# Kernel tuning notes

Measured on AMD Instinct MI355X. Metric: run time of the kernel, lower is better.

## Reference

```python
import jax, jax.numpy as jnp
import numpy as np

B, T, N, D, E = 16, 12, 512, 128, 32  # batch, time, nodes, model_dim, node_emb_dim


def setup_inputs() -> dict:
    key = jax.random.key(0)
    ks = jax.random.split(key, 7)
    return {
        "value": jax.random.normal(ks[0], (B, T, N, D), dtype=jnp.float32),
        "emb": jax.random.normal(ks[1], (T, N, E), dtype=jnp.float32),
        "attn_mask": jax.random.randint(ks[2], (B, N, N), 0, 2, dtype=jnp.int32),
        "W_qk": jax.random.normal(ks[3], (E, D), dtype=jnp.float32) * (1.0 / np.sqrt(E)),
        "b_qk": jax.random.normal(ks[4], (D,), dtype=jnp.float32) * 0.02,
        "W_v": jax.random.normal(ks[5], (D, D), dtype=jnp.float32) * (1.0 / np.sqrt(D)),
        "b_v": jax.random.normal(ks[6], (D,), dtype=jnp.float32) * 0.02,
    }


def reference(value, emb, attn_mask, W_qk, b_qk, W_v, b_v):
    # qk projection shared between query and key: [T, N, D]
    qk = emb @ W_qk + b_qk
    # query: softmax over feature dim D
    q = jax.nn.softmax(qk, axis=-1)                      # [T, N, D]
    # key: transpose then softmax over node dim N
    k = jax.nn.softmax(jnp.swapaxes(qk, -1, -2), axis=-1)  # [T, D, N]
    # value projection (note: out_proj in __init__ is unused in forward)
    v = value @ W_v + b_v                                # [B, T, N, D]
    # batch-independent base attention score, then broadcast over batch
    score = jnp.einsum('tnd,tdm->tnm', q, k)             # [T, N, N]
    score = jnp.broadcast_to(score[None], (value.shape[0],) + score.shape)  # [B, T, N, N]
    # masked fill: mask [B, N, N] -> [B, 1, N, N]
    score = jnp.where(attn_mask[:, None] == 0, jnp.float32(-1e9), score)
    out = jnp.einsum('btnm,btmd->btnd', score, v)         # [B, T, N, D]
    return out
```

## Files before the change

### kernel.cpp

```cpp
#include <hip/hip_runtime.h>

#define B_ 16
#define T_ 12
#define N_ 512
#define D_ 128
#define E_ 32

typedef __attribute__((ext_vector_type(8))) unsigned short u16x8;
typedef __attribute__((ext_vector_type(8))) __bf16 bf16x8;
typedef __attribute__((ext_vector_type(4))) float f32x4;

static __device__ __forceinline__ unsigned short f2bf(float f) {
    unsigned u = __float_as_uint(f);
    unsigned r = (u + 0x7fffu + ((u >> 16) & 1u)) >> 16;
    return (unsigned short)r;
}

static __device__ __forceinline__ void gld16(const void* src, void* dst) {
    __builtin_amdgcn_global_load_lds(
        (const __attribute__((address_space(1))) unsigned*)src,
        (__attribute__((address_space(3))) unsigned*)dst, 16, 0, 0);
}

__global__ __launch_bounds__(256) void k1(const float* __restrict__ emb,
                                          const float* __restrict__ Wqk,
                                          const float* __restrict__ bqk,
                                          unsigned short* __restrict__ qb,
                                          unsigned short* __restrict__ kN,
                                          const float* __restrict__ Wv,
                                          unsigned short* __restrict__ WvT,
                                          const int* __restrict__ mask,
                                          unsigned* __restrict__ mb) {
    __shared__ __align__(16) char LE[256 * 128];
    __shared__ float red[2][4][8];
    int hwid = blockIdx.x;
    int bid = (hwid & 7) * 144 + (hwid >> 3);
    int tid = threadIdx.x;

    if (bid < 192) {
        int t = bid >> 4;
        int d0 = (bid & 15) * 8;
        int dc = tid & 7, ni = tid >> 3;
        int wave = tid >> 6, lane = tid & 63;
        int l3 = lane >> 3, l7 = lane & 7;
        float wqv[E_];
#pragma unroll
        for (int e = 0; e < E_; ++e) wqv[e] = Wqk[e * D_ + d0 + dc];
        float bq = bqk[d0 + dc];
        const char* eb = (const char*)(emb + (size_t)t * N_ * E_);

        float vals[16];
#pragma unroll
        for (int pass = 0; pass < 2; ++pass) {
#pragma unroll
            for (int it = 0; it < 8; ++it) {
                int rl = it * 32 + wave * 8 + l3;
                int rg = pass * 256 + rl;
                gld16(eb + (size_t)rg * 128 + ((l7 * 16) ^ ((rg & 7) << 4)),
                      LE + (it * 32 + wave * 8) * 128 + lane * 16);
            }
            __syncthreads();
#pragma unroll
            for (int jj = 0; jj < 8; ++jj) {
                int n = pass * 256 + ni + 32 * jj;
                int nl = ni + 32 * jj;
                float a = bq;
#pragma unroll
                for (int s = 0; s < 8; ++s) {
                    f32x4 ev = *(const f32x4*)(LE + nl * 128 +
                                               ((s * 16) ^ ((n & 7) << 4)));
                    a = fmaf(ev[0], wqv[s * 4 + 0], a);
                    a = fmaf(ev[1], wqv[s * 4 + 1], a);
                    a = fmaf(ev[2], wqv[s * 4 + 2], a);
                    a = fmaf(ev[3], wqv[s * 4 + 3], a);
                }
                vals[pass * 8 + jj] = a;
            }
            __syncthreads();
        }

        float mx = -1e30f;
#pragma unroll
        for (int j = 0; j < 16; ++j) mx = fmaxf(mx, vals[j]);
#pragma unroll
        for (int s = 8; s < 64; s <<= 1) mx = fmaxf(mx, __shfl_xor(mx, s));
        int wv = tid >> 6;
        if ((tid & 63) < 8) red[0][wv][dc] = mx;
        __syncthreads();
        mx = fmaxf(fmaxf(red[0][0][dc], red[0][1][dc]),
                   fmaxf(red[0][2][dc], red[0][3][dc]));
        float sum = 0.f;
#pragma unroll
        for (int j = 0; j < 16; ++j) {
            vals[j] = __expf(vals[j] - mx);
            sum += vals[j];
        }
#pragma unroll
        for (int s = 8; s < 64; s <<= 1) sum += __shfl_xor(sum, s);
        if ((tid & 63) < 8) red[1][wv][dc] = sum;
        __syncthreads();
        sum = red[1][0][dc] + red[1][1][dc] + red[1][2][dc] + red[1][3][dc];
        float inv = 1.f / sum;
        unsigned short* op = kN + (size_t)t * N_ * D_ + d0 + dc;
#pragma unroll
        for (int j = 0; j < 16; ++j)
            op[(size_t)(ni + 32 * j) * D_] = f2bf(vals[j] * inv);
        return;
    }

    if (bid < 576) {
        int bid2 = bid - 192;
        int w = tid >> 6, l = tid & 63;
        float wq0[E_], wq1[E_];
#pragma unroll
        for (int e = 0; e < E_; ++e) {
            wq0[e] = Wqk[e * D_ + l];
            wq1[e] = Wqk[e * D_ + l + 64];
        }
        float b0 = bqk[l], b1 = bqk[l + 64];
        for (int rr = 0; rr < 4; ++rr) {
            int tn = bid2 * 16 + w * 4 + rr;
            const float* ep = emb + (size_t)tn * E_;
            float a0 = b0, a1 = b1;
#pragma unroll
            for (int e = 0; e < E_; ++e) {
                float ev = ep[e];
                a0 = fmaf(ev, wq0[e], a0);
                a1 = fmaf(ev, wq1[e], a1);
            }
            float mx = fmaxf(a0, a1);
#pragma unroll
            for (int s = 32; s > 0; s >>= 1) mx = fmaxf(mx, __shfl_xor(mx, s));
            float e0 = __expf(a0 - mx), e1 = __expf(a1 - mx);
            float sum = e0 + e1;
#pragma unroll
            for (int s = 32; s > 0; s >>= 1) sum += __shfl_xor(sum, s);
            float inv = 1.f / sum;
            qb[(size_t)tn * D_ + l] = f2bf(e0 * inv);
            qb[(size_t)tn * D_ + l + 64] = f2bf(e1 * inv);
        }
        return;
    }

    if (bid < 1088) {
        int o = (bid - 576) * 256 + tid;
        const int* mp = mask + (size_t)o * 32;
        unsigned bits = 0;
#pragma unroll
        for (int j = 0; j < 32; j += 4) {
            int4 m4 = *(const int4*)&mp[j];
            bits |= (m4.x ? 1u : 0u) << j;
            bits |= (m4.y ? 1u : 0u) << (j + 1);
            bits |= (m4.z ? 1u : 0u) << (j + 2);
            bits |= (m4.w ? 1u : 0u) << (j + 3);
        }
        mb[o] = bits;
        return;
    }

    {
        int i = (bid - 1088) * 256 + tid;
        int d = i >> 7, k = i & 127;
        WvT[d * 128 + k] = f2bf(Wv[k * 128 + d]);
    }
}

__global__ __launch_bounds__(256, 2) void kF(const unsigned short* __restrict__ qb,
                                             const unsigned short* __restrict__ kN,
                                             unsigned short* __restrict__ sc,
                                             const float* __restrict__ value,
                                             const unsigned short* __restrict__ WvT,
                                             const float* __restrict__ bv,
                                             unsigned short* __restrict__ vT) {
    __shared__ __align__(16) char LA[2][128 * 128];
    __shared__ __align__(16) char LB[2][128 * 128];
    int hwid = blockIdx.x;
    int bid = (hwid & 7) * 120 + (hwid >> 3);
    int tid = threadIdx.x;
    int wave = tid >> 6, lane = tid & 63;
    int q = lane >> 4, lr = lane & 15;
    int rbase = (wave & 1) * 64, cbase = (wave >> 1) * 64;
    int l3 = lane >> 3, l7 = lane & 7;

    f32x4 acc[4][4];
#pragma unroll
    for (int i = 0; i < 4; ++i)
#pragma unroll
        for (int j = 0; j < 4; ++j) acc[i][j] = (f32x4){0.f, 0.f, 0.f, 0.f};

#define STAGE_T(gbase, lb, c)                                                   \
    _Pragma("unroll") for (int it_ = 0; it_ < 4; ++it_) {                       \
        int row_ = it_ * 32 + wave * 8 + l3;                                    \
        gld16((gbase) + (size_t)row_ * 256 + (c) * 128 +                        \
                  ((l7 * 16) ^ ((row_ & 7) << 4)),                              \
              (lb) + (it_ * 32 + wave * 8) * 128 + lane * 16);                  \
    }

#define MFMA_CHUNK(c)                                                           \
    _Pragma("unroll") for (int ksl_ = 0; ksl_ < 2; ++ksl_) {                    \
        bf16x8 a_[4], b_[4];                                                    \
        _Pragma("unroll") for (int i_ = 0; i_ < 4; ++i_) {                      \
            int r_ = rbase + 16 * i_ + lr;                                      \
            a_[i_] = *(const bf16x8*)(LA[c] + r_ * 128 +                        \
                                      ((ksl_ * 64 + q * 16) ^ ((r_ & 7) << 4)));\
        }                                                                       \
        _Pragma("unroll") for (int j_ = 0; j_ < 4; ++j_) {                      \
            int r_ = cbase + 16 * j_ + lr;                                      \
            b_[j_] = *(const bf16x8*)(LB[c] + r_ * 128 +                        \
                                      ((ksl_ * 64 + q * 16) ^ ((r_ & 7) << 4)));\
        }                                                                       \
        _Pragma("unroll") for (int i_ = 0; i_ < 4; ++i_)                        \
            _Pragma("unroll") for (int j_ = 0; j_ < 4; ++j_)                    \
                acc[i_][j_] = __builtin_amdgcn_mfma_f32_16x16x32_bf16(          \
                    a_[i_], b_[j_], acc[i_][j_], 0, 0, 0);                      \
    }

    if (bid < 192) {
        int mt = bid & 3, nt = (bid >> 2) & 3, t = bid >> 4;
        int n0 = nt * 128, m0 = mt * 128;
        const char* qp = (const char*)(qb + (size_t)t * N_ * D_ + (size_t)n0 * D_);
        const char* kp = (const char*)(kN + (size_t)t * N_ * D_ + (size_t)m0 * D_);
        STAGE_T(qp, LA[0], 0)
        STAGE_T(kp, LB[0], 0)
        STAGE_T(qp, LA[1], 1)
        STAGE_T(kp, LB[1], 1)
        asm volatile("s_waitcnt vmcnt(8)" ::: "memory");
        __builtin_amdgcn_sched_barrier(0);
        __builtin_amdgcn_s_barrier();
        __builtin_amdgcn_sched_barrier(0);
        MFMA_CHUNK(0)
        asm volatile("s_waitcnt vmcnt(0)" ::: "memory");
        __builtin_amdgcn_sched_barrier(0);
        __builtin_amdgcn_s_barrier();
        __builtin_amdgcn_sched_barrier(0);
        MFMA_CHUNK(1)

        unsigned short* sp = sc + (size_t)t * N_ * N_;
#pragma unroll
        for (int i = 0; i < 4; ++i)
#pragma unroll
            for (int j = 0; j < 4; ++j) {
                int row0 = n0 + rbase + 16 * i + q * 4;
                int col = m0 + cbase + 16 * j + lr;
#pragma unroll
                for (int e = 0; e < 4; ++e)
                    sp[(size_t)(row0 + e) * N_ + col] = f2bf(acc[i][j][e]);
            }
        return;
    }

    {
        int idx = bid - 192;
        int mt = idx & 3, bt = idx >> 2;
        int m0 = mt * 128;
        const float* vp = value + ((size_t)bt * N_ + m0) * D_;
        const char* wp = (const char*)WvT;
        int g = tid >> 4, c16 = tid & 15;

        float4 v0[8], v1[8];
#pragma unroll
        for (int jj = 0; jj < 8; ++jj)
            v0[jj] = *(const float4*)(vp + (size_t)(g * 8 + jj) * D_ + c16 * 4);
        __builtin_amdgcn_sched_barrier(0);
        STAGE_T(wp, LA[0], 0)
        __builtin_amdgcn_sched_barrier(0);
#pragma unroll
        for (int jj = 0; jj < 8; ++jj)
            v1[jj] = *(const float4*)(vp + (size_t)(g * 8 + jj) * D_ + 64 + c16 * 4);
        __builtin_amdgcn_sched_barrier(0);
        STAGE_T(wp, LA[1], 1)
        __builtin_amdgcn_sched_barrier(0);

#pragma unroll
        for (int jj = 0; jj < 8; ++jj) {
            int row = g * 8 + jj;
            ushort4 o;
            o.x = f2bf(v0[jj].x); o.y = f2bf(v0[jj].y);
            o.z = f2bf(v0[jj].z); o.w = f2bf(v0[jj].w);
            *(ushort4*)(LB[0] + row * 128 + ((c16 * 8) ^ ((row & 7) << 4))) = o;
        }
        asm volatile("s_waitcnt vmcnt(12) lgkmcnt(0)" ::: "memory");
        __builtin_amdgcn_sched_barrier(0);
        __builtin_amdgcn_s_barrier();
        __builtin_amdgcn_sched_barrier(0);
        MFMA_CHUNK(0)
#pragma unroll
        for (int jj = 0; jj < 8; ++jj) {
            int row = g * 8 + jj;
            ushort4 o;
            o.x = f2bf(v1[jj].x); o.y = f2bf(v1[jj].y);
            o.z = f2bf(v1[jj].z); o.w = f2bf(v1[jj].w);
            *(ushort4*)(LB[1] + row * 128 + ((c16 * 8) ^ ((row & 7) << 4))) = o;
        }
        asm volatile("s_waitcnt vmcnt(0) lgkmcnt(0)" ::: "memory");
        __builtin_amdgcn_sched_barrier(0);
        __builtin_amdgcn_s_barrier();
        __builtin_amdgcn_sched_barrier(0);
        MFMA_CHUNK(1)

        unsigned short* op = vT + (size_t)bt * N_ * D_;
#pragma unroll
        for (int i = 0; i < 4; ++i) {
            int row0 = rbase + 16 * i + q * 4;
            float4 bq = *(const float4*)&bv[row0];
#pragma unroll
            for (int j = 0; j < 4; ++j) {
                int col = m0 + cbase + 16 * j + lr;
                op[(size_t)(row0 + 0) * N_ + col] = f2bf(acc[i][j][0] + bq.x);
                op[(size_t)(row0 + 1) * N_ + col] = f2bf(acc[i][j][1] + bq.y);
                op[(size_t)(row0 + 2) * N_ + col] = f2bf(acc[i][j][2] + bq.z);
                op[(size_t)(row0 + 3) * N_ + col] = f2bf(acc[i][j][3] + bq.w);
            }
        }
    }
#undef STAGE_T
#undef MFMA_CHUNK
}

__global__ __launch_bounds__(256, 3) void kC(const unsigned short* __restrict__ sc,
                                             const unsigned* __restrict__ mb,
                                             const unsigned short* __restrict__ vT,
                                             float* __restrict__ out) {
    int hwid = blockIdx.x;
    int w = (hwid & 7) * 96 + (hwid >> 3);
    int n0 = (w & 3) * 128;
    int r = w >> 2;
    int t = r % T_, b = r / T_;
    int tid = threadIdx.x;
    int wave = tid >> 6, lane = tid & 63;
    int q = lane >> 4, lr = lane & 15;
    int rbase = (wave & 1) * 64, cbase = (wave >> 1) * 64;

    __shared__ unsigned short Sb[128 * 64];
    __shared__ unsigned short Vb[2][128 * 64];

    const unsigned short* scp = sc + (size_t)t * N_ * N_ + (size_t)n0 * N_;
    const unsigned short* vtp = vT + ((size_t)(b * T_ + t)) * N_ * D_;
    const unsigned* mbp = mb + ((size_t)b * N_ + n0) * 16;
    const unsigned short NEG = 0xCE6E;

    f32x4 acc[4][4];
#pragma unroll
    for (int i = 0; i < 4; ++i)
#pragma unroll
        for (int j = 0; j < 4; ++j) acc[i][j] = (f32x4){0.f, 0.f, 0.f, 0.f};

    int sr = tid >> 1, sh2 = tid & 1;
    const unsigned short* sg = scp + (size_t)sr * N_ + sh2 * 32;
    const unsigned* mwp = mbp + sr * 16 + sh2;
    int swz_r = (sr & 7) << 4;
    char* Sw[4];
#pragma unroll
    for (int p = 0; p < 4; ++p)
        Sw[p] = (char*)Sb + sr * 128 + ((sh2 * 64 + p * 16) ^ swz_r);

    int l3 = lane >> 3, l7 = lane & 7;
    int vin = (l7 * 16) ^ (l3 << 4);
    const char* vbase = (const char*)vtp;

#pragma unroll
    for (int it = 0; it < 4; ++it) {
        int row = (it * 4 + wave) * 8 + l3;
        const char* src = vbase + (size_t)row * 1024 + vin;
        char* dst = (char*)&Vb[0][0] + ((it * 4 + wave) * 64 + lane) * 16;
        gld16(src, dst);
    }
    u16x8 sreg[4];
    unsigned mw;
#pragma unroll
    for (int p = 0; p < 4; ++p) sreg[p] = *(const u16x8*)(sg + p * 8);
    mw = mwp[0];

    for (int kc = 0; kc < 8; ++kc) {
        int cur = kc & 1;
#pragma unroll
        for (int p = 0; p < 4; ++p) {
            unsigned bits = mw >> (p * 8);
            u16x8 o;
#pragma unroll
            for (int j = 0; j < 8; ++j)
                o[j] = ((bits >> j) & 1u) ? sreg[p][j] : NEG;
            *(u16x8*)Sw[p] = o;
        }
        if (kc < 7) {
            int off = (kc + 1) * 128;
#pragma unroll
            for (int it = 0; it < 4; ++it) {
                int row = (it * 4 + wave) * 8 + l3;
                const char* src = vbase + (size_t)row * 1024 + off + vin;
                char* dst = (char*)&Vb[cur ^ 1][0] + ((it * 4 + wave) * 64 + lane) * 16;
                gld16(src, dst);
            }
            int eoff = (kc + 1) * 64;
#pragma unroll
            for (int p = 0; p < 4; ++p) sreg[p] = *(const u16x8*)(sg + eoff + p * 8);
            mw = mwp[(kc + 1) * 2];
        }
        asm volatile("s_waitcnt lgkmcnt(0)" ::: "memory");
        __builtin_amdgcn_s_barrier();
        __builtin_amdgcn_sched_barrier(0);
        {
            const char* Sbase = (const char*)Sb;
            const char* Vbase = (const char*)&Vb[cur][0];
            int swz_l = (lr & 7) << 4;
#pragma unroll
            for (int ks = 0; ks < 2; ++ks) {
                bf16x8 a[4], bb[4];
#pragma unroll
                for (int i = 0; i < 4; ++i) {
                    int rr = rbase + 16 * i + lr;
                    a[i] = *(const bf16x8*)(Sbase + rr * 128 + ((ks * 64 + q * 16) ^ swz_l));
                }
#pragma unroll
                for (int j = 0; j < 4; ++j) {
                    int d = cbase + 16 * j + lr;
                    bb[j] = *(const bf16x8*)(Vbase + d * 128 + ((ks * 64 + q * 16) ^ swz_l));
                }
#pragma unroll
                for (int i = 0; i < 4; ++i)
#pragma unroll
                    for (int j = 0; j < 4; ++j)
                        acc[i][j] = __builtin_amdgcn_mfma_f32_16x16x32_bf16(
                            a[i], bb[j], acc[i][j], 0, 0, 0);
            }
        }
        __builtin_amdgcn_s_barrier();
        __builtin_amdgcn_sched_barrier(0);
    }

    float* ob = out + ((size_t)(b * T_ + t)) * N_ * D_;
#pragma unroll
    for (int i = 0; i < 4; ++i) {
#pragma unroll
        for (int j = 0; j < 4; ++j) {
            int row0 = n0 + rbase + 16 * i + q * 4;
            int col = cbase + 16 * j + lr;
#pragma unroll
            for (int e = 0; e < 4; ++e)
                ob[(size_t)(row0 + e) * D_ + col] = acc[i][j][e];
        }
    }
}

extern "C" void kernel_launch(void* const* d_in, const int* in_sizes, int n_in,
                              void* d_out, int out_size, void* d_ws, size_t ws_size,
                              hipStream_t stream) {
    const float* value = (const float*)d_in[0];
    const float* emb   = (const float*)d_in[1];
    const int*   mask  = (const int*)d_in[2];
    const float* Wqk   = (const float*)d_in[3];
    const float* bqk   = (const float*)d_in[4];
    const float* Wv    = (const float*)d_in[5];
    const float* bvv   = (const float*)d_in[6];
    float* out = (float*)d_out;

    float* ws = (float*)d_ws;
    unsigned short* qb   = (unsigned short*)(ws + 786432);
    unsigned short* kNb  = (unsigned short*)(ws + 1179648);
    unsigned short* scb  = (unsigned short*)(ws + 1572864);
    unsigned short* vtb  = (unsigned short*)(ws + 3145728);
    unsigned short* WvTb = (unsigned short*)(ws + 9437184);
    unsigned*       mbp  = (unsigned*)(ws + 9445376);

    k1<<<1152, 256, 0, stream>>>(emb, Wqk, bqk, qb, kNb, Wv, WvTb, mask, mbp);
    kF<<<960, 256, 0, stream>>>(qb, kNb, scb, value, WvTb, bvv, vtb);
    kC<<<768, 256, 0, stream>>>(scb, mbp, vtb, out);
}
```

Before: 157.6 us.

## Double-buffer score tile and prefetch two stages ahead in kC

Double-buffers the masked score tile in LDS and loads score and mask registers two chunks ahead. The mask merge for the next chunk now runs after the current chunk's MFMAs, leaving one barrier per iteration instead of two. Explicit vmcnt waits replace full drains, and the loop is fully unrolled. LDS per block grows and occupancy is lowered from 3 to 2 blocks per SIMD group, which trades latency hiding across blocks for overlap within a block.

```diff
diff --git a/kernel.cpp b/kernel.cpp
--- a/kernel.cpp
+++ b/kernel.cpp
@@ -317,7 +317,7 @@
 #undef MFMA_CHUNK
 }
 
-__global__ __launch_bounds__(256, 3) void kC(const unsigned short* __restrict__ sc,
+__global__ __launch_bounds__(256, 2) void kC(const unsigned short* __restrict__ sc,
                                              const unsigned* __restrict__ mb,
                                              const unsigned short* __restrict__ vT,
                                              float* __restrict__ out) {
@@ -331,8 +331,8 @@
     int q = lane >> 4, lr = lane & 15;
     int rbase = (wave & 1) * 64, cbase = (wave >> 1) * 64;
 
-    __shared__ unsigned short Sb[128 * 64];
-    __shared__ unsigned short Vb[2][128 * 64];
+    __shared__ __align__(16) unsigned short Sb[2][128 * 64];
+    __shared__ __align__(16) unsigned short Vb[2][128 * 64];
 
     const unsigned short* scp = sc + (size_t)t * N_ * N_ + (size_t)n0 * N_;
     const unsigned short* vtp = vT + ((size_t)(b * T_ + t)) * N_ * D_;
@@ -349,84 +349,96 @@
     const unsigned short* sg = scp + (size_t)sr * N_ + sh2 * 32;
     const unsigned* mwp = mbp + sr * 16 + sh2;
     int swz_r = (sr & 7) << 4;
-    char* Sw[4];
-#pragma unroll
-    for (int p = 0; p < 4; ++p)
-        Sw[p] = (char*)Sb + sr * 128 + ((sh2 * 64 + p * 16) ^ swz_r);
 
     int l3 = lane >> 3, l7 = lane & 7;
     int vin = (l7 * 16) ^ (l3 << 4);
     const char* vbase = (const char*)vtp;
 
-#pragma unroll
-    for (int it = 0; it < 4; ++it) {
-        int row = (it * 4 + wave) * 8 + l3;
-        const char* src = vbase + (size_t)row * 1024 + vin;
-        char* dst = (char*)&Vb[0][0] + ((it * 4 + wave) * 64 + lane) * 16;
-        gld16(src, dst);
-    }
-    u16x8 sreg[4];
-    unsigned mw;
-#pragma unroll
-    for (int p = 0; p < 4; ++p) sreg[p] = *(const u16x8*)(sg + p * 8);
-    mw = mwp[0];
-
+    u16x8 sreg[2][4];
+    unsigned mwv[2];
+
+#define VISS(buf, kc)                                                           \
+    _Pragma("unroll") for (int it_ = 0; it_ < 4; ++it_) {                       \
+        int row_ = (it_ * 4 + wave) * 8 + l3;                                   \
+        gld16(vbase + (size_t)row_ * 1024 + (kc) * 128 + vin,                   \
+              (char*)Vb[buf] + ((it_ * 4 + wave) * 64 + lane) * 16);            \
+    }
+
+#define SLOAD(s, kc)                                                            \
+    _Pragma("unroll") for (int p_ = 0; p_ < 4; ++p_)                            \
+        sreg[s][p_] = *(const u16x8*)(sg + (kc) * 64 + p_ * 8);                 \
+    mwv[s] = mwp[(kc) * 2];
+
+#define MERGE(buf, s)                                                           \
+    _Pragma("unroll") for (int p_ = 0; p_ < 4; ++p_) {                          \
+        unsigned bits_ = mwv[s] >> (p_ * 8);                                    \
+        u16x8 o_;                                                               \
+        _Pragma("unroll") for (int j_ = 0; j_ < 8; ++j_)                        \
+            o_[j_] = ((bits_ >> j_) & 1u) ? sreg[s][p_][j_] : NEG;              \
+        *(u16x8*)((char*)Sb[buf] + sr * 128 + ((sh2 * 64 + p_ * 16) ^ swz_r)) = \
+            o_;                                                                 \
+    }
+
+#define MFMAC(c)                                                                \
+    {                                                                           \
+        const char* Sbase_ = (const char*)Sb[c];                                \
+        const char* Vbase_ = (const char*)Vb[c];                                \
+        int swz_l_ = (lr & 7) << 4;                                             \
+        _Pragma("unroll") for (int ks_ = 0; ks_ < 2; ++ks_) {                   \
+            bf16x8 a_[4], bb_[4];                                               \
+            _Pragma("unroll") for (int i_ = 0; i_ < 4; ++i_) {                  \
+                int r_ = rbase + 16 * i_ + lr;                                  \
+                a_[i_] = *(const bf16x8*)(Sbase_ + r_ * 128 +                   \
+                                          ((ks_ * 64 + q * 16) ^ swz_l_));      \
+            }                                                                   \
+            _Pragma("unroll") for (int j_ = 0; j_ < 4; ++j_) {                  \
+                int d_ = cbase + 16 * j_ + lr;                                  \
+                bb_[j_] = *(const bf16x8*)(Vbase_ + d_ * 128 +                  \
+                                           ((ks_ * 64 + q * 16) ^ swz_l_));     \
+            }                                                                   \
+            _Pragma("unroll") for (int i_ = 0; i_ < 4; ++i_)                    \
+                _Pragma("unroll") for (int j_ = 0; j_ < 4; ++j_)                \
+                    acc[i_][j_] = __builtin_amdgcn_mfma_f32_16x16x32_bf16(      \
+                        a_[i_], bb_[j_], acc[i_][j_], 0, 0, 0);                 \
+        }                                                                       \
+    }
+
+    VISS(0, 0)
+    SLOAD(0, 0)
+    SLOAD(1, 1)
+    asm volatile("s_waitcnt vmcnt(5)" ::: "memory");
+    __builtin_amdgcn_sched_barrier(0);
+    MERGE(0, 0)
+    asm volatile("s_waitcnt lgkmcnt(0)" ::: "memory");
+    __builtin_amdgcn_s_barrier();
+    __builtin_amdgcn_sched_barrier(0);
+
+#pragma unroll
     for (int kc = 0; kc < 8; ++kc) {
-        int cur = kc & 1;
-#pragma unroll
-        for (int p = 0; p < 4; ++p) {
-            unsigned bits = mw >> (p * 8);
-            u16x8 o;
-#pragma unroll
-            for (int j = 0; j < 8; ++j)
-                o[j] = ((bits >> j) & 1u) ? sreg[p][j] : NEG;
-            *(u16x8*)Sw[p] = o;
-        }
+        int cur = kc & 1, nxt = cur ^ 1;
+        if (kc < 7) { VISS(nxt, kc + 1) }
+        if (kc < 6) { SLOAD(cur, kc + 2) }
+        if (kc < 6) {
+            asm volatile("s_waitcnt vmcnt(9)" ::: "memory");
+        } else if (kc == 6) {
+            asm volatile("s_waitcnt vmcnt(4)" ::: "memory");
+        } else {
+            asm volatile("s_waitcnt vmcnt(0)" ::: "memory");
+        }
+        __builtin_amdgcn_sched_barrier(0);
+        MFMAC(cur)
+        if (kc < 7) { MERGE(nxt, nxt) }
+        asm volatile("s_waitcnt lgkmcnt(0)" ::: "memory");
         if (kc < 7) {
-            int off = (kc + 1) * 128;
-#pragma unroll
-            for (int it = 0; it < 4; ++it) {
-                int row = (it * 4 + wave) * 8 + l3;
-                const char* src = vbase + (size_t)row * 1024 + off + vin;
-                char* dst = (char*)&Vb[cur ^ 1][0] + ((it * 4 + wave) * 64 + lane) * 16;
-                gld16(src, dst);
-            }
-            int eoff = (kc + 1) * 64;
-#pragma unroll
-            for (int p = 0; p < 4; ++p) sreg[p] = *(const u16x8*)(sg + eoff + p * 8);
-            mw = mwp[(kc + 1) * 2];
-        }
-        asm volatile("s_waitcnt lgkmcnt(0)" ::: "memory");
-        __builtin_amdgcn_s_barrier();
-        __builtin_amdgcn_sched_barrier(0);
-        {
-            const char* Sbase = (const char*)Sb;
-            const char* Vbase = (const char*)&Vb[cur][0];
-            int swz_l = (lr & 7) << 4;
-#pragma unroll
-            for (int ks = 0; ks < 2; ++ks) {
-                bf16x8 a[4], bb[4];
-#pragma unroll
-                for (int i = 0; i < 4; ++i) {
-                    int rr = rbase + 16 * i + lr;
-                    a[i] = *(const bf16x8*)(Sbase + rr * 128 + ((ks * 64 + q * 16) ^ swz_l));
-                }
-#pragma unroll
-                for (int j = 0; j < 4; ++j) {
-                    int d = cbase + 16 * j + lr;
-                    bb[j] = *(const bf16x8*)(Vbase + d * 128 + ((ks * 64 + q * 16) ^ swz_l));
-                }
-#pragma unroll
-                for (int i = 0; i < 4; ++i)
-#pragma unroll
-                    for (int j = 0; j < 4; ++j)
-                        acc[i][j] = __builtin_amdgcn_mfma_f32_16x16x32_bf16(
-                            a[i], bb[j], acc[i][j], 0, 0, 0);
-            }
-        }
-        __builtin_amdgcn_s_barrier();
-        __builtin_amdgcn_sched_barrier(0);
-    }
+            __builtin_amdgcn_s_barrier();
+            __builtin_amdgcn_sched_barrier(0);
+        }
+    }
+
+#undef VISS
+#undef SLOAD
+#undef MERGE
+#undef MFMAC
 
     float* ob = out + ((size_t)(b * T_ + t)) * N_ * D_;
 #pragma unroll
```

Result: no change. 159.7 us (+1.4%).
